# Performance work log

Measured on AMD Instinct MI355X. Metric: run time of the kernel, lower is better.

The kernel has to match this reference:

```python
import jax, jax.numpy as jnp
import numpy as np

B, N, D = 1, 4096, 320
HEADS, DIM_HEAD = 8, 40
PHASE, Hm, Wm = 3, 64, 64  # guidance mask spatial dims; Hm*Wm == N


def setup_inputs() -> dict:
    key = jax.random.key(0)
    ks = jax.random.split(key, 7)
    s = 0.02
    x = jax.random.normal(ks[0], (B, N, D), jnp.float32)
    guidance_mask = jax.random.bernoulli(ks[1], 0.25, (B, PHASE, Hm, Wm)).astype(jnp.float32)
    Wq = jax.random.normal(ks[2], (D, HEADS * DIM_HEAD), jnp.float32) * s
    Wk = jax.random.normal(ks[3], (D, HEADS * DIM_HEAD), jnp.float32) * s
    Wv = jax.random.normal(ks[4], (D, HEADS * DIM_HEAD), jnp.float32) * s
    Wo = jax.random.normal(ks[5], (HEADS * DIM_HEAD, D), jnp.float32) * s
    bo = jnp.zeros((D,), jnp.float32)
    return {"x": x, "guidance_mask": guidance_mask, "Wq": Wq, "Wk": Wk,
            "Wv": Wv, "Wo": Wo, "bo": bo}


def reference(x, guidance_mask, Wq, Wk, Wv, Wo, bo):
    b, n, _ = x.shape
    h, dh = HEADS, DIM_HEAD
    scale = dh ** (-0.5)

    def split_heads(t):
        # b n (h d) -> (b h) n d
        return t.reshape(b, n, h, dh).transpose(0, 2, 1, 3).reshape(b * h, n, dh)

    q = split_heads(x @ Wq)
    k = split_heads(x @ Wk)
    v = split_heads(x @ Wv)

    sim = jnp.einsum('bid,bjd->bij', q, k) * scale  # (b*h, n, n)

    _, p, Hh, Ww = guidance_mask.shape
    HW = Hh * Ww  # == n
    g = guidance_mask.reshape(b, p, HW)
    # sum over phases of outer products, clamped at 1 (binary block mask)
    mask_sim = jnp.minimum(jnp.einsum('bpi,bpj->bij', g, g), 1.0)  # (b, HW, HW)
    mask_sim = jnp.repeat(mask_sim, h, axis=0)  # (b*h, HW, HW), heads within each b

    neg = -jnp.finfo(sim.dtype).max
    # original: sim[:, :, :HW][mask_sim == 0] = -max ; here n == HW so full matrix
    sim = jnp.where(mask_sim == 0, neg, sim)

    attn = jax.nn.softmax(sim, axis=-1)
    out = jnp.einsum('bij,bjd->bid', attn, v)  # (b*h, n, dh)
    out = out.reshape(b, h, n, dh).transpose(0, 2, 1, 3).reshape(b, n, h * dh)
    return out @ Wo + bo
```

## Files before the change

kernel.cpp:

```cpp
#include <hip/hip_runtime.h>
#include <hip/hip_bf16.h>
#include <stdint.h>

#define NT 4096
#define DM 320
#define NH 8
#define DH 40
#define KS 4
#define QSCALE 0.22811013f
#define PSTR 68
#define KFJB 640

typedef float f32x4 __attribute__((ext_vector_type(4)));
typedef __bf16 bf16x8 __attribute__((ext_vector_type(8)));

__device__ __forceinline__ unsigned short f2b(float f) {
  unsigned u = __builtin_bit_cast(unsigned, f);
  u += 0x7FFFu + ((u >> 16) & 1u);
  return (unsigned short)(u >> 16);
}

__device__ __forceinline__ bf16x8 ld_bf8(const unsigned short* p) {
  uint4 v = *(const uint4*)p;
  return __builtin_bit_cast(bf16x8, v);
}

__device__ __forceinline__ f32x4 mfma16(bf16x8 a, bf16x8 b, f32x4 c) {
  return __builtin_amdgcn_mfma_f32_16x16x32_bf16(a, b, c, 0, 0, 0);
}

__device__ __forceinline__ float fexp2(float x) {
#if __has_builtin(__builtin_amdgcn_exp2f)
  return __builtin_amdgcn_exp2f(x);
#else
  float r; asm("v_exp_f32 %0, %1" : "=v"(r) : "v"(x)); return r;
#endif
}

__device__ __forceinline__ uint2 pack4(float a, float b, float c, float d) {
  uint2 pk;
  pk.x = (unsigned)f2b(a) | ((unsigned)f2b(b) << 16);
  pk.y = (unsigned)f2b(c) | ((unsigned)f2b(d) << 16);
  return pk;
}

__device__ __forceinline__ size_t fmi(int tile, int nk, int k, int o) {
  return ((size_t)tile * nk + (k >> 5)) * 512 + (size_t)((k >> 3) & 3) * 128 +
         (size_t)(o & 15) * 8 + (k & 7);
}

__global__ __launch_bounds__(256) void prep_kernel(
    const float* __restrict__ x, const float* __restrict__ g,
    const float* __restrict__ Wq, const float* __restrict__ Wk,
    const float* __restrict__ Wv, const float* __restrict__ Wo,
    unsigned short* __restrict__ xbf, unsigned char* __restrict__ sgp,
    unsigned short* __restrict__ Wtf, int* __restrict__ perm,
    int* __restrict__ invp, int* __restrict__ nqp) {
  const int b = blockIdx.x, t = threadIdx.x;
  if (b == 100) {
    __shared__ int cnt[256];
    unsigned char mys[16];
    int c1 = 0;
#pragma unroll
    for (int i = 0; i < 16; ++i) {
      int tok = t * 16 + i;
      unsigned s = 0;
      if (g[tok] != 0.f)          s |= 1u;
      if (g[NT + tok] != 0.f)     s |= 2u;
      if (g[2 * NT + tok] != 0.f) s |= 4u;
      mys[i] = (unsigned char)s;
      c1 += (s != 0u);
    }
    cnt[t] = c1;
    __syncthreads();
    for (int off = 1; off < 256; off <<= 1) {
      int v = (t >= off) ? cnt[t - off] : 0;
      __syncthreads();
      cnt[t] += v;
      __syncthreads();
    }
    const int nq = cnt[255];
    int p1 = cnt[t] - c1;
    int p0 = nq + (t * 16 - p1);
#pragma unroll
    for (int i = 0; i < 16; ++i) {
      int tok = t * 16 + i;
      if (mys[i] != 0) { perm[p1] = tok; invp[tok] = p1; sgp[p1] = mys[i]; p1++; }
      else             { perm[p0] = tok; invp[tok] = p0; sgp[p0] = 0;      p0++; }
    }
    if (t == 0) nqp[0] = nq;
    return;
  }
  if (b > 100) {
    int base = (b - 101) * 2560;
#pragma unroll
    for (int j = 0; j < 10; ++j) {
      int i = (base + j * 256 + t) * 4;
      int m = i / DM, k = i % DM;
      float4 v = *(const float4*)(x + i);
      ushort4 u;
      u.x = f2b(v.x); u.y = f2b(v.y); u.z = f2b(v.z); u.w = f2b(v.w);
      *(ushort4*)(xbf + fmi(m >> 4, 10, k, m)) = u;
    }
    return;
  }
  __shared__ __align__(16) unsigned short lt[64 * 72];
  int kx = b % 5, cy = b / 5;
  int cm = cy % 5;
  const float* src;
  int rowbase;
  if (cy < 5)       { src = Wq; rowbase = cm * 64; }
  else if (cy < 10) { src = Wk; rowbase = 320 + cm * 64; }
  else if (cy < 15) { src = Wv; rowbase = 640 + cm * 64; }
  else              { src = Wo; rowbase = 960 + cm * 64; }
  const int c0 = cm * 64;
  const int k0 = kx * 64;
#pragma unroll
  for (int i = 0; i < 4; ++i) {
    int kr = (t >> 4) + i * 16, cc = (t & 15) * 4;
    float4 w4 = *(const float4*)&src[(size_t)(k0 + kr) * DM + c0 + cc];
    lt[(cc + 0) * 72 + kr] = f2b(w4.x);
    lt[(cc + 1) * 72 + kr] = f2b(w4.y);
    lt[(cc + 2) * 72 + kr] = f2b(w4.z);
    lt[(cc + 3) * 72 + kr] = f2b(w4.w);
  }
  __syncthreads();
#pragma unroll
  for (int i = 0; i < 2; ++i) {
    int idx = t + i * 256, cl = idx >> 3, ch = idx & 7;
    int c = rowbase + cl, k = k0 + ch * 8;
    *(uint4*)&Wtf[fmi(c >> 4, 10, k, c)] = *(const uint4*)&lt[cl * 72 + ch * 8];
  }
}

__global__ __launch_bounds__(256, 4) void qkv_gemm(
    const unsigned short* __restrict__ xbf, const unsigned short* __restrict__ Wtf,
    const int* __restrict__ invp,
    unsigned short* __restrict__ Qb, unsigned short* __restrict__ Kf,
    unsigned short* __restrict__ Vf) {
  const int t = threadIdx.x;
  const int w = t >> 6, lane = t & 63, quad = lane >> 4, ln = lane & 15;
  const int m0 = blockIdx.x * 64;
  const int cy = blockIdx.y;
  const int a = cy / 5;
  const int cc0 = (cy % 5) * 64;
  const int mt = (m0 >> 4) + w;
  const int ct0 = a * 20 + (cc0 >> 4);

  f32x4 acc[4] = {{0,0,0,0},{0,0,0,0},{0,0,0,0},{0,0,0,0}};
  for (int kc = 0; kc < 10; ++kc) {
    bf16x8 xf = ld_bf8(xbf + ((size_t)(mt * 10 + kc)) * 512 + lane * 8);
#pragma unroll
    for (int nt = 0; nt < 4; ++nt) {
      bf16x8 wf = ld_bf8(Wtf + ((size_t)((ct0 + nt) * 10 + kc)) * 512 + lane * 8);
      if (a < 2) acc[nt] = mfma16(wf, xf, acc[nt]);
      else       acc[nt] = mfma16(xf, wf, acc[nt]);
    }
  }
  if (a == 0) {
    const int bp = invp[m0 + w * 16 + ln];
#pragma unroll
    for (int nt = 0; nt < 4; ++nt) {
      int c = cc0 + nt * 16 + quad * 4;
      int h = c / DH, d = c % DH;
      uint2 pk = pack4(acc[nt][0] * QSCALE, acc[nt][1] * QSCALE,
                       acc[nt][2] * QSCALE, acc[nt][3] * QSCALE);
      *(uint2*)&Qb[((size_t)h * NT + bp) * 64 + d] = pk;
    }
  } else if (a == 1) {
    const int bp = invp[m0 + w * 16 + ln];
#pragma unroll
    for (int nt = 0; nt < 4; ++nt) {
      int c = cc0 + nt * 16 + quad * 4;
      int h = c / DH, d = c % DH;
      uint2 pk = pack4(acc[nt][0], acc[nt][1], acc[nt][2], acc[nt][3]);
      size_t base = ((size_t)h * 256 + (bp >> 4)) * KFJB;
      size_t idx = (d < 32)
          ? base + (size_t)(d >> 3) * 128 + (size_t)(bp & 15) * 8 + (d & 7)
          : base + 512 + (size_t)(bp & 15) * 8 + (d - 32);
      *(uint2*)&Kf[idx] = pk;
    }
  } else {
    const int mb = m0 + w * 16 + quad * 4;
    int bpr[4];
#pragma unroll
    for (int r = 0; r < 4; ++r) bpr[r] = invp[mb + r];
#pragma unroll
    for (int nt = 0; nt < 4; ++nt) {
      int c = cc0 + nt * 16 + ln;
      int h = c / DH, d = c % DH;
#pragma unroll
      for (int r = 0; r < 4; ++r) {
        int bp = bpr[r];
        size_t idx = ((((((size_t)(h * 64 + (bp >> 6)) * 3 + (d >> 4)) * 2 +
                         ((bp >> 5) & 1)) * 4 + ((bp >> 3) & 3)) * 16 + (d & 15))) * 8 +
                     (bp & 7);
        Vf[idx] = f2b(acc[nt][r]);
      }
    }
  }
}

__global__ __launch_bounds__(256, 4) void attn_kernel(
    const unsigned short* __restrict__ Qb, const unsigned short* __restrict__ Kf,
    const unsigned short* __restrict__ Vf, const unsigned char* __restrict__ sgp,
    const int* __restrict__ perm, const int* __restrict__ nqp,
    unsigned short* __restrict__ Opf, float* __restrict__ Lpart) {
  __shared__ __align__(16) unsigned short pt[4][32 * PSTR];
  const int t = threadIdx.x;
  const int w = t >> 6, lane = t & 63, quad = lane >> 4, ln = lane & 15;
  const int h = blockIdx.y, sp = blockIdx.z;
  const int qt = (blockIdx.x + 8 * sp) & 31;
  const int qrow = qt * 128 + w * 32;
  const int nq = nqp[0];
  const int nkt = (nq + 63) >> 6;
  const int nq_pad = (nq + 127) & ~127;
  const bool writer = (qt * 128 >= nq_pad);
  const int jt_end = (!writer && (qt + 1) * 128 <= nq) ? nkt : 64;

  const unsigned short* Kfh = Kf + (size_t)h * 256 * KFJB;
  const unsigned short* Vfh = Vf + (size_t)h * 196608;
  unsigned short* ptw = pt[w];
  const uint4 z4 = {0, 0, 0, 0};
  const uint4 ones4 = {0x3F803F80u, 0x3F803F80u, 0x3F803F80u, 0x3F803F80u};
  const bf16x8 onesb = __builtin_bit_cast(bf16x8, ones4);
  const bool vone = (ln == 8);

  bf16x8 qa[2][2];
  unsigned sqx4[2], uqx4[2];
  int morig[2];
  f32x4 o[3][2] = {{{0,0,0,0},{0,0,0,0}},{{0,0,0,0},{0,0,0,0}},{{0,0,0,0},{0,0,0,0}}};

#pragma unroll
  for (int tq = 0; tq < 2; ++tq) {
    int bp = qrow + tq * 16 + ln;
    morig[tq] = perm[bp];
    if (!writer) {
      const unsigned short* Qp = Qb + ((size_t)h * NT + bp) * 64;
      qa[tq][0] = ld_bf8(Qp + quad * 8);
      uint4 q1 = z4;
      if (quad == 0) q1 = *(const uint4*)(Qp + 32);
      qa[tq][1] = __builtin_bit_cast(bf16x8, q1);
      unsigned s = sgp[bp];
      sqx4[tq] = s * 0x01010101u;
      uqx4[tq] = (s == 0u) ? 0xFFFFFFFFu : 0u;
      if (s == 0u) {
        qa[tq][0] = __builtin_bit_cast(bf16x8, z4);
        qa[tq][1] = __builtin_bit_cast(bf16x8, z4);
      }
    }
  }

  for (int jt = sp; jt < jt_end; jt += KS) {
    if (!writer) {
      uint4 kfr0[4], kfr1[4];
#pragma unroll
      for (int nt = 0; nt < 4; ++nt) {
        const unsigned short* kb = Kfh + (size_t)(jt * 4 + nt) * KFJB;
        kfr0[nt] = *(const uint4*)(kb + lane * 8);
        kfr1[nt] = z4;
        if (lane < 16) kfr1[nt] = *(const uint4*)(kb + 512 + lane * 8);
      }
#pragma unroll
      for (int nt = 0; nt < 4; ++nt) {
        bf16x8 ka0 = __builtin_bit_cast(bf16x8, kfr0[nt]);
        bf16x8 ka1 = __builtin_bit_cast(bf16x8, kfr1[nt]);
        unsigned spj = *(const unsigned*)(sgp + jt * 64 + nt * 16 + quad * 4);
#pragma unroll
        for (int tq = 0; tq < 2; ++tq) {
          f32x4 acc = {0.f, 0.f, 0.f, 0.f};
          acc = mfma16(ka0, qa[tq][0], acc);
          acc = mfma16(ka1, qa[tq][1], acc);
          unsigned m4 = (spj & sqx4[tq]) | uqx4[tq];
          unsigned u[4];
#pragma unroll
          for (int r = 0; r < 4; ++r) {
            unsigned mb = (m4 >> (8 * r)) & 255u;
            float am = mb ? acc[r] : -3.0e38f;
            u[r] = __builtin_bit_cast(unsigned, fexp2(am));
          }
          uint2 pk;
          pk.x = (u[0] >> 16) | (u[1] & 0xffff0000u);
          pk.y = (u[2] >> 16) | (u[3] & 0xffff0000u);
          *(uint2*)&ptw[(tq * 16 + ln) * PSTR + nt * 16 + quad * 4] = pk;
        }
      }
    }
    uint4 vfr[6];
#pragma unroll
    for (int ot = 0; ot < 3; ++ot)
#pragma unroll
      for (int c = 0; c < 2; ++c)
        vfr[ot * 2 + c] =
            *(const uint4*)(Vfh + ((size_t)((jt * 3 + ot) * 2 + c)) * 512 + lane * 8);
    if (vone) { vfr[4] = ones4; vfr[5] = ones4; }

    bf16x8 pb[2][2];
    if (!writer) {
      asm volatile("s_waitcnt lgkmcnt(0)" ::: "memory");
#pragma unroll
      for (int tq = 0; tq < 2; ++tq) {
        pb[tq][0] = ld_bf8(&ptw[(tq * 16 + ln) * PSTR + quad * 8]);
        pb[tq][1] = ld_bf8(&ptw[(tq * 16 + ln) * PSTR + 32 + quad * 8]);
      }
    } else {
      pb[0][0] = onesb; pb[0][1] = onesb; pb[1][0] = onesb; pb[1][1] = onesb;
    }
#pragma unroll
    for (int ot = 0; ot < 3; ++ot) {
      bf16x8 va0 = __builtin_bit_cast(bf16x8, vfr[ot * 2]);
      bf16x8 va1 = __builtin_bit_cast(bf16x8, vfr[ot * 2 + 1]);
#pragma unroll
      for (int tq = 0; tq < 2; ++tq) {
        o[ot][tq] = mfma16(va0, pb[tq][0], o[ot][tq]);
        o[ot][tq] = mfma16(va1, pb[tq][1], o[ot][tq]);
      }
    }
  }

#pragma unroll
  for (int tq = 0; tq < 2; ++tq) {
    int m = morig[tq];
#pragma unroll
    for (int ot = 0; ot < 3; ++ot) {
      int d0 = ot * 16 + quad * 4;
      if (d0 < DH) {
        int c = h * DH + d0;
        uint2 pk = pack4(o[ot][tq][0], o[ot][tq][1], o[ot][tq][2], o[ot][tq][3]);
        *(uint2*)&Opf[fmi(sp * 256 + (m >> 4), 10, c, m)] = pk;
      }
    }
    if (quad == 2)
      Lpart[sp * NT + m] = o[2][tq][0];
  }
}

__global__ __launch_bounds__(256, 4) void out_gemm(
    const unsigned short* __restrict__ Opf, const float* __restrict__ Lpart,
    const unsigned short* __restrict__ Wtf, const float* __restrict__ bo,
    float* __restrict__ out) {
  const int t = threadIdx.x;
  const int w = t >> 6, lane = t & 63, quad = lane >> 4, ln = lane & 15;
  const int m0 = blockIdx.x * 64;
  const int cc0 = blockIdx.y * 64;
  const int mt = (m0 >> 4) + w;
  const int m = m0 + w * 16 + ln;
  const int ct0 = 60 + (cc0 >> 4);
  float ls = 0.f;
#pragma unroll
  for (int sp = 0; sp < KS; ++sp) ls += Lpart[sp * NT + m];
  const float inv = 1.f / ls;

  f32x4 acc[4] = {{0,0,0,0},{0,0,0,0},{0,0,0,0},{0,0,0,0}};
  for (int kc = 0; kc < 10; ++kc) {
    float s8[8] = {0, 0, 0, 0, 0, 0, 0, 0};
#pragma unroll
    for (int sp = 0; sp < KS; ++sp) {
      uint4 v = *(const uint4*)(Opf + ((size_t)((sp * 256 + mt) * 10 + kc)) * 512 +
                                lane * 8);
      unsigned vv[4] = {v.x, v.y, v.z, v.w};
#pragma unroll
      for (int j = 0; j < 4; ++j) {
        s8[2 * j]     += __builtin_bit_cast(float, vv[j] << 16);
        s8[2 * j + 1] += __builtin_bit_cast(float, vv[j] & 0xffff0000u);
      }
    }
    unsigned short af8[8];
#pragma unroll
    for (int j = 0; j < 8; ++j) af8[j] = f2b(s8[j] * inv);
    bf16x8 af = ld_bf8(af8);
#pragma unroll
    for (int nt = 0; nt < 4; ++nt) {
      bf16x8 wf = ld_bf8(Wtf + ((size_t)((ct0 + nt) * 10 + kc)) * 512 + lane * 8);
      acc[nt] = mfma16(wf, af, acc[nt]);
    }
  }
#pragma unroll
  for (int nt = 0; nt < 4; ++nt) {
    int c = cc0 + nt * 16 + quad * 4;
    float4 bv = *(const float4*)(bo + c);
    float4 ov;
    ov.x = acc[nt][0] + bv.x;
    ov.y = acc[nt][1] + bv.y;
    ov.z = acc[nt][2] + bv.z;
    ov.w = acc[nt][3] + bv.w;
    *(float4*)(out + (size_t)m * DM + c) = ov;
  }
}

extern "C" void kernel_launch(void* const* d_in, const int* in_sizes, int n_in,
                              void* d_out, int out_size, void* d_ws, size_t ws_size,
                              hipStream_t stream) {
  const float* x  = (const float*)d_in[0];
  const float* g  = (const float*)d_in[1];
  const float* Wq = (const float*)d_in[2];
  const float* Wk = (const float*)d_in[3];
  const float* Wv = (const float*)d_in[4];
  const float* Wo = (const float*)d_in[5];
  const float* bo = (const float*)d_in[6];
  float* out = (float*)d_out;

  char* ws = (char*)d_ws;
  const size_t SGP_OFF  = 0;
  const size_t NQ_OFF   = 4096;
  const size_t PERM_OFF = 8192;
  const size_t INV_OFF  = 24576;
  const size_t XBF_OFF  = 40960;
  const size_t WTF_OFF = XBF_OFF + (size_t)NT * DM * 2;
  const size_t QB_OFF  = WTF_OFF + (size_t)1280 * DM * 2;
  const size_t KF_OFF  = QB_OFF + (size_t)NH * NT * 64 * 2;
  const size_t VF_OFF  = KF_OFF + (size_t)NH * 256 * KFJB * 2;
  const size_t OPF_OFF = VF_OFF + (size_t)NH * 196608 * 2;
  const size_t LP_OFF  = OPF_OFF + (size_t)KS * 256 * 10 * 512 * 2;
  unsigned char* sgp   = (unsigned char*)(ws + SGP_OFF);
  int* nqp             = (int*)(ws + NQ_OFF);
  int* perm            = (int*)(ws + PERM_OFF);
  int* invp            = (int*)(ws + INV_OFF);
  unsigned short* xbf  = (unsigned short*)(ws + XBF_OFF);
  unsigned short* Wtf  = (unsigned short*)(ws + WTF_OFF);
  unsigned short* Qb   = (unsigned short*)(ws + QB_OFF);
  unsigned short* Kf   = (unsigned short*)(ws + KF_OFF);
  unsigned short* Vf   = (unsigned short*)(ws + VF_OFF);
  unsigned short* Opf  = (unsigned short*)(ws + OPF_OFF);
  float* Lpart         = (float*)(ws + LP_OFF);

  prep_kernel<<<229, 256, 0, stream>>>(x, g, Wq, Wk, Wv, Wo, xbf, sgp, Wtf,
                                       perm, invp, nqp);
  qkv_gemm<<<dim3(64, 15), 256, 0, stream>>>(xbf, Wtf, invp, Qb, Kf, Vf);
  attn_kernel<<<dim3(32, NH, KS), 256, 0, stream>>>(Qb, Kf, Vf, sgp, perm, nqp,
                                                    Opf, Lpart);
  out_gemm<<<dim3(64, 5), 256, 0, stream>>>(Opf, Lpart, Wtf, bo, out);
}
```

Before: 139.5 us.

## Compute uniform-attention rows once as per-head V mean instead of per query

Queries whose guidance mask is empty get uniform attention over all keys, so their output is just the mean of V. Previously every such query tile was run through the full key loop with a ones matrix for P. Now one extra block per head computes the V column mean, those query tiles exit early, and out_gemm swaps in the mean for rows whose permuted index is at or past nq. Partially filled tiles now stop at nkt instead of looping over all key tiles. The trade-off is an extra reduction block, an extra branch and load in out_gemm, and reads of stale Lpart for rows whose result is discarded anyway.

```diff
diff --git a/kernel.cpp b/kernel.cpp
--- a/kernel.cpp
+++ b/kernel.cpp
@@ -205,29 +205,60 @@
     const unsigned short* __restrict__ Qb, const unsigned short* __restrict__ Kf,
     const unsigned short* __restrict__ Vf, const unsigned char* __restrict__ sgp,
     const int* __restrict__ perm, const int* __restrict__ nqp,
-    unsigned short* __restrict__ Opf, float* __restrict__ Lpart) {
+    unsigned short* __restrict__ Opf, float* __restrict__ Lpart,
+    unsigned short* __restrict__ Ubf) {
   __shared__ __align__(16) unsigned short pt[4][32 * PSTR];
+  __shared__ float vs[4][48];
   const int t = threadIdx.x;
   const int w = t >> 6, lane = t & 63, quad = lane >> 4, ln = lane & 15;
   const int h = blockIdx.y, sp = blockIdx.z;
-  const int qt = (blockIdx.x + 8 * sp) & 31;
-  const int qrow = qt * 128 + w * 32;
   const int nq = nqp[0];
   const int nkt = (nq + 63) >> 6;
   const int nq_pad = (nq + 127) & ~127;
-  const bool writer = (qt * 128 >= nq_pad);
-  const int jt_end = (!writer && (qt + 1) * 128 <= nq) ? nkt : 64;
-
-  const unsigned short* Kfh = Kf + (size_t)h * 256 * KFJB;
+
   const unsigned short* Vfh = Vf + (size_t)h * 196608;
-  unsigned short* ptw = pt[w];
   const uint4 z4 = {0, 0, 0, 0};
   const uint4 ones4 = {0x3F803F80u, 0x3F803F80u, 0x3F803F80u, 0x3F803F80u};
   const bf16x8 onesb = __builtin_bit_cast(bf16x8, ones4);
+
+  if (blockIdx.x == 32) {
+    if (sp != 0) return;
+    f32x4 o[3] = {{0,0,0,0},{0,0,0,0},{0,0,0,0}};
+    for (int jt = w; jt < 64; jt += 4) {
+#pragma unroll
+      for (int ot = 0; ot < 3; ++ot) {
+        uint4 v0 = *(const uint4*)(Vfh + ((size_t)((jt * 3 + ot) * 2 + 0)) * 512 +
+                                   lane * 8);
+        uint4 v1 = *(const uint4*)(Vfh + ((size_t)((jt * 3 + ot) * 2 + 1)) * 512 +
+                                   lane * 8);
+        o[ot] = mfma16(__builtin_bit_cast(bf16x8, v0), onesb, o[ot]);
+        o[ot] = mfma16(__builtin_bit_cast(bf16x8, v1), onesb, o[ot]);
+      }
+    }
+    if (ln == 0) {
+#pragma unroll
+      for (int ot = 0; ot < 3; ++ot)
+#pragma unroll
+        for (int r = 0; r < 4; ++r) vs[w][ot * 16 + quad * 4 + r] = o[ot][r];
+    }
+    __syncthreads();
+    if (t < DH) {
+      float s = vs[0][t] + vs[1][t] + vs[2][t] + vs[3][t];
+      Ubf[h * DH + t] = f2b(s * (1.0f / (float)NT));
+    }
+    return;
+  }
+
+  const int qt = (blockIdx.x + 8 * sp) & 31;
+  if (qt * 128 >= nq_pad) return;
+  const int qrow = qt * 128 + w * 32;
+
+  const unsigned short* Kfh = Kf + (size_t)h * 256 * KFJB;
+  unsigned short* ptw = pt[w];
   const bool vone = (ln == 8);
 
   bf16x8 qa[2][2];
-  unsigned sqx4[2], uqx4[2];
+  unsigned sqx4[2];
   int morig[2];
   f32x4 o[3][2] = {{{0,0,0,0},{0,0,0,0}},{{0,0,0,0},{0,0,0,0}},{{0,0,0,0},{0,0,0,0}}};
 
@@ -235,55 +266,45 @@
   for (int tq = 0; tq < 2; ++tq) {
     int bp = qrow + tq * 16 + ln;
     morig[tq] = perm[bp];
-    if (!writer) {
-      const unsigned short* Qp = Qb + ((size_t)h * NT + bp) * 64;
-      qa[tq][0] = ld_bf8(Qp + quad * 8);
-      uint4 q1 = z4;
-      if (quad == 0) q1 = *(const uint4*)(Qp + 32);
-      qa[tq][1] = __builtin_bit_cast(bf16x8, q1);
-      unsigned s = sgp[bp];
-      sqx4[tq] = s * 0x01010101u;
-      uqx4[tq] = (s == 0u) ? 0xFFFFFFFFu : 0u;
-      if (s == 0u) {
-        qa[tq][0] = __builtin_bit_cast(bf16x8, z4);
-        qa[tq][1] = __builtin_bit_cast(bf16x8, z4);
-      }
-    }
-  }
-
-  for (int jt = sp; jt < jt_end; jt += KS) {
-    if (!writer) {
-      uint4 kfr0[4], kfr1[4];
-#pragma unroll
-      for (int nt = 0; nt < 4; ++nt) {
-        const unsigned short* kb = Kfh + (size_t)(jt * 4 + nt) * KFJB;
-        kfr0[nt] = *(const uint4*)(kb + lane * 8);
-        kfr1[nt] = z4;
-        if (lane < 16) kfr1[nt] = *(const uint4*)(kb + 512 + lane * 8);
-      }
-#pragma unroll
-      for (int nt = 0; nt < 4; ++nt) {
-        bf16x8 ka0 = __builtin_bit_cast(bf16x8, kfr0[nt]);
-        bf16x8 ka1 = __builtin_bit_cast(bf16x8, kfr1[nt]);
-        unsigned spj = *(const unsigned*)(sgp + jt * 64 + nt * 16 + quad * 4);
-#pragma unroll
-        for (int tq = 0; tq < 2; ++tq) {
-          f32x4 acc = {0.f, 0.f, 0.f, 0.f};
-          acc = mfma16(ka0, qa[tq][0], acc);
-          acc = mfma16(ka1, qa[tq][1], acc);
-          unsigned m4 = (spj & sqx4[tq]) | uqx4[tq];
-          unsigned u[4];
-#pragma unroll
-          for (int r = 0; r < 4; ++r) {
-            unsigned mb = (m4 >> (8 * r)) & 255u;
-            float am = mb ? acc[r] : -3.0e38f;
-            u[r] = __builtin_bit_cast(unsigned, fexp2(am));
-          }
-          uint2 pk;
-          pk.x = (u[0] >> 16) | (u[1] & 0xffff0000u);
-          pk.y = (u[2] >> 16) | (u[3] & 0xffff0000u);
-          *(uint2*)&ptw[(tq * 16 + ln) * PSTR + nt * 16 + quad * 4] = pk;
+    const unsigned short* Qp = Qb + ((size_t)h * NT + bp) * 64;
+    qa[tq][0] = ld_bf8(Qp + quad * 8);
+    uint4 q1 = z4;
+    if (quad == 0) q1 = *(const uint4*)(Qp + 32);
+    qa[tq][1] = __builtin_bit_cast(bf16x8, q1);
+    sqx4[tq] = (unsigned)sgp[bp] * 0x01010101u;
+  }
+
+  for (int jt = sp; jt < nkt; jt += KS) {
+    uint4 kfr0[4], kfr1[4];
+#pragma unroll
+    for (int nt = 0; nt < 4; ++nt) {
+      const unsigned short* kb = Kfh + (size_t)(jt * 4 + nt) * KFJB;
+      kfr0[nt] = *(const uint4*)(kb + lane * 8);
+      kfr1[nt] = z4;
+      if (lane < 16) kfr1[nt] = *(const uint4*)(kb + 512 + lane * 8);
+    }
+#pragma unroll
+    for (int nt = 0; nt < 4; ++nt) {
+      bf16x8 ka0 = __builtin_bit_cast(bf16x8, kfr0[nt]);
+      bf16x8 ka1 = __builtin_bit_cast(bf16x8, kfr1[nt]);
+      unsigned spj = *(const unsigned*)(sgp + jt * 64 + nt * 16 + quad * 4);
+#pragma unroll
+      for (int tq = 0; tq < 2; ++tq) {
+        f32x4 acc = {0.f, 0.f, 0.f, 0.f};
+        acc = mfma16(ka0, qa[tq][0], acc);
+        acc = mfma16(ka1, qa[tq][1], acc);
+        unsigned m4 = spj & sqx4[tq];
+        unsigned u[4];
+#pragma unroll
+        for (int r = 0; r < 4; ++r) {
+          unsigned mb = (m4 >> (8 * r)) & 255u;
+          float am = mb ? acc[r] : -3.0e38f;
+          u[r] = __builtin_bit_cast(unsigned, fexp2(am));
         }
+        uint2 pk;
+        pk.x = (u[0] >> 16) | (u[1] & 0xffff0000u);
+        pk.y = (u[2] >> 16) | (u[3] & 0xffff0000u);
+        *(uint2*)&ptw[(tq * 16 + ln) * PSTR + nt * 16 + quad * 4] = pk;
       }
     }
     uint4 vfr[6];
@@ -296,15 +317,11 @@
     if (vone) { vfr[4] = ones4; vfr[5] = ones4; }
 
     bf16x8 pb[2][2];
-    if (!writer) {
-      asm volatile("s_waitcnt lgkmcnt(0)" ::: "memory");
-#pragma unroll
-      for (int tq = 0; tq < 2; ++tq) {
-        pb[tq][0] = ld_bf8(&ptw[(tq * 16 + ln) * PSTR + quad * 8]);
-        pb[tq][1] = ld_bf8(&ptw[(tq * 16 + ln) * PSTR + 32 + quad * 8]);
-      }
-    } else {
-      pb[0][0] = onesb; pb[0][1] = onesb; pb[1][0] = onesb; pb[1][1] = onesb;
+    asm volatile("s_waitcnt lgkmcnt(0)" ::: "memory");
+#pragma unroll
+    for (int tq = 0; tq < 2; ++tq) {
+      pb[tq][0] = ld_bf8(&ptw[(tq * 16 + ln) * PSTR + quad * 8]);
+      pb[tq][1] = ld_bf8(&ptw[(tq * 16 + ln) * PSTR + 32 + quad * 8]);
     }
 #pragma unroll
     for (int ot = 0; ot < 3; ++ot) {
@@ -338,7 +355,8 @@
 __global__ __launch_bounds__(256, 4) void out_gemm(
     const unsigned short* __restrict__ Opf, const float* __restrict__ Lpart,
     const unsigned short* __restrict__ Wtf, const float* __restrict__ bo,
-    float* __restrict__ out) {
+    const int* __restrict__ invp, const int* __restrict__ nqp,
+    const unsigned short* __restrict__ Ubf, float* __restrict__ out) {
   const int t = threadIdx.x;
   const int w = t >> 6, lane = t & 63, quad = lane >> 4, ln = lane & 15;
   const int m0 = blockIdx.x * 64;
@@ -346,6 +364,7 @@
   const int mt = (m0 >> 4) + w;
   const int m = m0 + w * 16 + ln;
   const int ct0 = 60 + (cc0 >> 4);
+  const bool uni = invp[m] >= nqp[0];
   float ls = 0.f;
 #pragma unroll
   for (int sp = 0; sp < KS; ++sp) ls += Lpart[sp * NT + m];
@@ -353,6 +372,7 @@
 
   f32x4 acc[4] = {{0,0,0,0},{0,0,0,0},{0,0,0,0},{0,0,0,0}};
   for (int kc = 0; kc < 10; ++kc) {
+    uint4 uv = *(const uint4*)(Ubf + kc * 32 + quad * 8);
     float s8[8] = {0, 0, 0, 0, 0, 0, 0, 0};
 #pragma unroll
     for (int sp = 0; sp < KS; ++sp) {
@@ -365,10 +385,13 @@
         s8[2 * j + 1] += __builtin_bit_cast(float, vv[j] & 0xffff0000u);
       }
     }
-    unsigned short af8[8];
-#pragma unroll
-    for (int j = 0; j < 8; ++j) af8[j] = f2b(s8[j] * inv);
-    bf16x8 af = ld_bf8(af8);
+    uint4 av;
+    av.x = (unsigned)f2b(s8[0] * inv) | ((unsigned)f2b(s8[1] * inv) << 16);
+    av.y = (unsigned)f2b(s8[2] * inv) | ((unsigned)f2b(s8[3] * inv) << 16);
+    av.z = (unsigned)f2b(s8[4] * inv) | ((unsigned)f2b(s8[5] * inv) << 16);
+    av.w = (unsigned)f2b(s8[6] * inv) | ((unsigned)f2b(s8[7] * inv) << 16);
+    if (uni) av = uv;
+    bf16x8 af = __builtin_bit_cast(bf16x8, av);
 #pragma unroll
     for (int nt = 0; nt < 4; ++nt) {
       bf16x8 wf = ld_bf8(Wtf + ((size_t)((ct0 + nt) * 10 + kc)) * 512 + lane * 8);
@@ -412,6 +435,7 @@
   const size_t VF_OFF  = KF_OFF + (size_t)NH * 256 * KFJB * 2;
   const size_t OPF_OFF = VF_OFF + (size_t)NH * 196608 * 2;
   const size_t LP_OFF  = OPF_OFF + (size_t)KS * 256 * 10 * 512 * 2;
+  const size_t UBF_OFF = LP_OFF + (size_t)KS * NT * 4;
   unsigned char* sgp   = (unsigned char*)(ws + SGP_OFF);
   int* nqp             = (int*)(ws + NQ_OFF);
   int* perm            = (int*)(ws + PERM_OFF);
@@ -423,11 +447,13 @@
   unsigned short* Vf   = (unsigned short*)(ws + VF_OFF);
   unsigned short* Opf  = (unsigned short*)(ws + OPF_OFF);
   float* Lpart         = (float*)(ws + LP_OFF);
+  unsigned short* Ubf  = (unsigned short*)(ws + UBF_OFF);
 
   prep_kernel<<<229, 256, 0, stream>>>(x, g, Wq, Wk, Wv, Wo, xbf, sgp, Wtf,
                                        perm, invp, nqp);
   qkv_gemm<<<dim3(64, 15), 256, 0, stream>>>(xbf, Wtf, invp, Qb, Kf, Vf);
-  attn_kernel<<<dim3(32, NH, KS), 256, 0, stream>>>(Qb, Kf, Vf, sgp, perm, nqp,
-                                                    Opf, Lpart);
-  out_gemm<<<dim3(64, 5), 256, 0, stream>>>(Opf, Lpart, Wtf, bo, out);
-}
+  attn_kernel<<<dim3(33, NH, KS), 256, 0, stream>>>(Qb, Kf, Vf, sgp, perm, nqp,
+                                                    Opf, Lpart, Ubf);
+  out_gemm<<<dim3(64, 5), 256, 0, stream>>>(Opf, Lpart, Wtf, bo, invp, nqp,
+                                            Ubf, out);
+}
```

New measurement: 135.8 us. 2.6% less time.
